# Optimization experiments

Hardware: AMD Instinct MI355X
Metric: run time of the kernel (lower is better)

Reference implementation:

```python
import jax, jax.numpy as jnp
import numpy as np
import math

D_MODEL = 1024
N_HEADS = 16
SLOT_DIM = 64
N_SLOTS = 1024
TOP_K = 2
LN_EPS = 1e-5


def setup_inputs() -> dict:
    key = jax.random.key(0)
    ks = jax.random.split(key, 8)
    x = jax.random.normal(ks[0], (4, 2048, D_MODEL), dtype=jnp.float32)
    ln_gamma = jnp.ones((D_MODEL,), jnp.float32)
    ln_beta = jnp.zeros((D_MODEL,), jnp.float32)
    q_w = jax.random.normal(ks[1], (N_HEADS * SLOT_DIM, D_MODEL), jnp.float32) / math.sqrt(D_MODEL)
    q_b = jnp.zeros((N_HEADS * SLOT_DIM,), jnp.float32)
    slot_signatures = jax.random.normal(ks[2], (N_HEADS, N_SLOTS, SLOT_DIM), jnp.float32) * 0.5
    slot_values = jax.random.normal(ks[3], (N_HEADS, N_SLOTS, SLOT_DIM), jnp.float32) * 0.02
    out_w = jax.random.normal(ks[4], (D_MODEL, N_HEADS * SLOT_DIM), jnp.float32) / math.sqrt(N_HEADS * SLOT_DIM)
    out_b = jnp.zeros((D_MODEL,), jnp.float32)
    temperature = jnp.ones((1,), jnp.float32)
    return {"x": x, "ln_gamma": ln_gamma, "ln_beta": ln_beta, "q_w": q_w, "q_b": q_b,
            "slot_signatures": slot_signatures, "slot_values": slot_values,
            "out_w": out_w, "out_b": out_b, "temperature": temperature}


def _ternary_ste(sig):
    # forward = {-1,0,+1} quantization; backward = identity (straight-through)
    q = jnp.where(sig > 0.3, 1.0, jnp.where(sig < -0.3, -1.0, 0.0))
    return sig + jax.lax.stop_gradient(q - sig)


def reference(x, ln_gamma, ln_beta, q_w, q_b, slot_signatures, slot_values, out_w, out_b, temperature):
    B, T, D = x.shape
    # LayerNorm
    mean = jnp.mean(x, axis=-1, keepdims=True)
    var = jnp.var(x, axis=-1, keepdims=True)
    x_norm = (x - mean) * jax.lax.rsqrt(var + LN_EPS) * ln_gamma + ln_beta
    # Query projection -> [B, T, H, slot_dim]
    q = (x_norm @ q_w.T + q_b).reshape(B, T, N_HEADS, SLOT_DIM)
    sigs = _ternary_ste(slot_signatures)  # [H, S, d]
    scores = jnp.einsum('bthd,hsd->bths', q, sigs)
    scores = scores / (temperature * math.sqrt(SLOT_DIM))  # [B, T, H, S]
    # top-k routing
    topk_scores, slot_idx = jax.lax.top_k(scores, TOP_K)  # [B, T, H, K]
    weights = jax.nn.softmax(topk_scores, axis=-1)
    # gather selected slot values: [B, T, H, K, d]
    h_idx = jnp.arange(N_HEADS)[None, None, :, None]
    selected = slot_values[h_idx, slot_idx]
    read = jnp.sum(selected * weights[..., None], axis=3)  # [B, T, H, d]
    read = read.reshape(B, T, N_HEADS * SLOT_DIM)
    out = read @ out_w.T + out_b
    return x + out
```

## Files before the change

### kernel.cpp

```cpp
#include <hip/hip_runtime.h>

typedef unsigned short u16;
typedef unsigned int   u32;
typedef float f32x4  __attribute__((ext_vector_type(4)));
typedef float f32x16 __attribute__((ext_vector_type(16)));
typedef __bf16 bf16x8 __attribute__((ext_vector_type(8)));

__device__ __forceinline__ u16 f2bf(float f){
  u32 u = __float_as_uint(f);
  u += 0x7fffu + ((u >> 16) & 1u);
  return (u16)(u >> 16);
}

__device__ __forceinline__ void gld16(const void* g, void* l){
  __builtin_amdgcn_global_load_lds((const __attribute__((address_space(1))) u32*)g,
                                   (__attribute__((address_space(3))) u32*)l, 16, 0, 0);
}

#define WAITCNT_VM0   0x0F70
#define WAITCNT_VM4   0x0F74
#define WAITCNT_LGKM0 0xC07F

__global__ __launch_bounds__(256) void convert_kernel(
    const float* __restrict__ qw, const float* __restrict__ ow,
    const float* __restrict__ sg,
    u16* __restrict__ qwb, u16* __restrict__ owb, u16* __restrict__ sgb){
  int i = (blockIdx.x * 256 + threadIdx.x) * 4;
  f32x4 a = *(const f32x4*)(qw + i);
  f32x4 b = *(const f32x4*)(ow + i);
  f32x4 s = *(const f32x4*)(sg + i);
  uint2 pa, pb, ps;
  pa.x = (u32)f2bf(a[0]) | ((u32)f2bf(a[1]) << 16);
  pa.y = (u32)f2bf(a[2]) | ((u32)f2bf(a[3]) << 16);
  pb.x = (u32)f2bf(b[0]) | ((u32)f2bf(b[1]) << 16);
  pb.y = (u32)f2bf(b[2]) | ((u32)f2bf(b[3]) << 16);
  float t0 = (s[0] > 0.3f) ? 1.0f : ((s[0] < -0.3f) ? -1.0f : 0.0f);
  float t1 = (s[1] > 0.3f) ? 1.0f : ((s[1] < -0.3f) ? -1.0f : 0.0f);
  float t2 = (s[2] > 0.3f) ? 1.0f : ((s[2] < -0.3f) ? -1.0f : 0.0f);
  float t3 = (s[3] > 0.3f) ? 1.0f : ((s[3] < -0.3f) ? -1.0f : 0.0f);
  ps.x = (u32)f2bf(t0) | ((u32)f2bf(t1) << 16);
  ps.y = (u32)f2bf(t2) | ((u32)f2bf(t3) << 16);
  *(uint2*)(qwb + i) = pa;
  *(uint2*)(owb + i) = pb;
  *(uint2*)(sgb + i) = ps;
}

__global__ __launch_bounds__(256) void ln_kernel(
    const float* __restrict__ x, const float* __restrict__ g,
    const float* __restrict__ b, u16* __restrict__ xn){
  const int tid = threadIdx.x, lane = tid & 63, w = tid >> 6;
  const int t = blockIdx.x * 4 + w;
  const float* xr = x + (size_t)t * 1024;
  f32x4 v[4];
  #pragma unroll
  for (int j = 0; j < 4; ++j) v[j] = *(const f32x4*)(xr + j * 256 + lane * 4);
  float s = 0.f, ss = 0.f;
  #pragma unroll
  for (int j = 0; j < 4; ++j)
    #pragma unroll
    for (int e = 0; e < 4; ++e){ s += v[j][e]; ss += v[j][e] * v[j][e]; }
  #pragma unroll
  for (int off = 32; off; off >>= 1){
    s  += __shfl_xor(s, off);
    ss += __shfl_xor(ss, off);
  }
  float mean = s * (1.0f / 1024.0f);
  float var  = ss * (1.0f / 1024.0f) - mean * mean;
  float rs   = rsqrtf(var + 1e-5f);
  #pragma unroll
  for (int j = 0; j < 4; ++j){
    f32x4 gv = *(const f32x4*)(g + j * 256 + lane * 4);
    f32x4 bv = *(const f32x4*)(b + j * 256 + lane * 4);
    float y0 = (v[j][0]-mean)*rs*gv[0]+bv[0];
    float y1 = (v[j][1]-mean)*rs*gv[1]+bv[1];
    float y2 = (v[j][2]-mean)*rs*gv[2]+bv[2];
    float y3 = (v[j][3]-mean)*rs*gv[3]+bv[3];
    uint2 pk;
    pk.x = (u32)f2bf(y0) | ((u32)f2bf(y1) << 16);
    pk.y = (u32)f2bf(y2) | ((u32)f2bf(y3) << 16);
    *(uint2*)(xn + (size_t)t * 1024 + j * 256 + lane * 4) = pk;
  }
}

__global__ __launch_bounds__(256, 2) void gemm_bt(
    const u16* __restrict__ A, const u16* __restrict__ B,
    const float* __restrict__ bias, const float* __restrict__ resid,
    float* __restrict__ outf, u16* __restrict__ outb, int mode){
  __shared__ u16 As[2][128 * 64];
  __shared__ u16 Bs[2][128 * 64];
  const int tid = threadIdx.x;
  const int b = blockIdx.x;
  const int m0 = ((b & 7) * 8 + ((b >> 3) & 7)) * 128;
  const int n0 = (b >> 6) * 128;
  const int w = tid >> 6, lane = tid & 63, lm = lane & 15, quad = lane >> 4;
  const int wm = (w & 1) * 64, wn = (w >> 1) * 64;
  const int lr = lane >> 3;
  const int lg = (lane & 7) ^ lr;
  const f32x4 fz = {0.f, 0.f, 0.f, 0.f};
  f32x4 acc[4][4];
  #pragma unroll
  for (int i = 0; i < 4; ++i)
    #pragma unroll
    for (int j = 0; j < 4; ++j) acc[i][j] = fz;

  const u16* gA = A + (size_t)(m0 + w * 32 + lr) * 1024 + lg * 8;
  const u16* gB = B + (size_t)(n0 + w * 32 + lr) * 1024 + lg * 8;
  const int lbase = (w * 32) * 64;
  const int sw = lm & 7;

  auto stage = [&](int kt, int bb){
    #pragma unroll
    for (int sub = 0; sub < 4; ++sub){
      gld16(gA + (size_t)(sub * 8) * 1024 + kt * 64, &As[bb][lbase + sub * 8 * 64]);
      gld16(gB + (size_t)(sub * 8) * 1024 + kt * 64, &Bs[bb][lbase + sub * 8 * 64]);
    }
  };

  stage(0, 0);
  for (int kt = 0; kt < 16; ++kt){
    __syncthreads();
    if (kt < 15) stage(kt + 1, (kt + 1) & 1);
    const u16* as = As[kt & 1];
    const u16* bs = Bs[kt & 1];
    #pragma unroll
    for (int kk = 0; kk < 2; ++kk){
      const int ch = ((quad + kk * 4) ^ sw) * 8;
      bf16x8 afr[4], bfr[4];
      #pragma unroll
      for (int i = 0; i < 4; ++i)
        afr[i] = *(const bf16x8*)(&as[(wm + i * 16 + lm) * 64 + ch]);
      #pragma unroll
      for (int j = 0; j < 4; ++j)
        bfr[j] = *(const bf16x8*)(&bs[(wn + j * 16 + lm) * 64 + ch]);
      #pragma unroll
      for (int i = 0; i < 4; ++i)
        #pragma unroll
        for (int j = 0; j < 4; ++j)
          acc[i][j] = __builtin_amdgcn_mfma_f32_16x16x32_bf16(afr[i], bfr[j], acc[i][j], 0, 0, 0);
    }
  }

  #pragma unroll
  for (int i = 0; i < 4; ++i){
    #pragma unroll
    for (int r = 0; r < 4; ++r){
      int grow = m0 + wm + i * 16 + quad * 4 + r;
      #pragma unroll
      for (int j = 0; j < 4; ++j){
        int gcol = n0 + wn + j * 16 + lm;
        float v = acc[i][j][r] + bias[gcol];
        if (mode){
          v += resid[(size_t)grow * 1024 + gcol];
          outf[(size_t)grow * 1024 + gcol] = v;
        } else {
          outb[(size_t)grow * 1024 + gcol] = f2bf(v);
        }
      }
    }
  }
}

#define MERGE2(V1,I1,V2,I2, o1,oi1,o2,oi2) {                      \
    u32   cb2 = (o2 > V2) ? oi2 : I2;                             \
    float c2  = fmaxf(V2, o2);                                    \
    u32   nb1 = (o1 > V1) ? oi1 : I1;                             \
    float n1  = fmaxf(V1, o1);                                    \
    float n2  = __builtin_amdgcn_fmed3f(V1, o1, c2);              \
    u32   nb2 = (n2 == o1) ? oi1 : ((n2 == V1) ? I1 : cb2);       \
    V1 = n1; I1 = nb1; V2 = n2; I2 = nb2; }

__global__ __launch_bounds__(256) void route_kernel(
    const u16* __restrict__ q, const u16* __restrict__ sig,
    const float* __restrict__ V, const float* __restrict__ temp,
    u16* __restrict__ rd){
  const int h = blockIdx.y;
  const int t0 = blockIdx.x * 64;
  const int tid = threadIdx.x, w = tid >> 6, lane = tid & 63;
  const int col = lane & 31, half = lane >> 5;

  __shared__ u16 sbuf[4][2][32 * 64];
  __shared__ float sv1[4][64], sv2[4][64];
  __shared__ u32   si1[4][64], si2[4][64];
  __shared__ float fw1[64], fw2[64];
  __shared__ int   fi1[64], fi2[64];

  const u16* q0 = q + (size_t)(t0 + col) * 1024 + h * 64 + half * 8;
  bf16x8 qa[4], qb[4];
  #pragma unroll
  for (int c = 0; c < 4; ++c){
    qa[c] = *(const bf16x8*)(q0 + c * 16);
    qb[c] = *(const bf16x8*)(q0 + 32 * 1024 + c * 16);
  }
  __builtin_amdgcn_s_waitcnt(WAITCNT_VM0);

  const int lr = lane >> 3, lg = (lane & 7) ^ lr;
  const u16* ssrc = sig + (size_t)h * 65536 + (size_t)(w * 256 + lr) * 64 + lg * 8;
  auto stage = [&](int i, int bb){
    const u16* s0 = ssrc + (size_t)i * 32 * 64;
    u16* d0 = &sbuf[w][bb][0];
    #pragma unroll
    for (int sub = 0; sub < 4; ++sub)
      gld16(s0 + sub * 8 * 64, d0 + sub * 8 * 64);
  };

  int p[4];
  #pragma unroll
  for (int c = 0; c < 4; ++c) p[c] = col * 64 + (((2 * c + half) ^ (col & 7)) * 8);

  const f32x16 fzero = {};
  float v1a = -3.0e38f, v2a = -3.0e38f, v1b = -3.0e38f, v2b = -3.0e38f;
  u32 b1a = 0, b2a = 0, b1b = 0, b2b = 0;

  stage(0, 0);
  stage(1, 1);
  #pragma unroll
  for (int i = 0; i < 8; ++i){
    if (i < 7) __builtin_amdgcn_s_waitcnt(WAITCNT_VM4);
    else       __builtin_amdgcn_s_waitcnt(WAITCNT_VM0);
    const u16* buf = sbuf[w][i & 1];
    bf16x8 sf0 = *(const bf16x8*)(&buf[p[0]]);
    bf16x8 sf1 = *(const bf16x8*)(&buf[p[1]]);
    bf16x8 sf2 = *(const bf16x8*)(&buf[p[2]]);
    bf16x8 sf3 = *(const bf16x8*)(&buf[p[3]]);
    __builtin_amdgcn_s_waitcnt(WAITCNT_LGKM0);
    if (i < 6) stage(i + 2, i & 1);
    u32 bt = (u32)i;
    #pragma unroll
    for (int set = 0; set < 2; ++set){
      f32x16 acc;
      acc = __builtin_amdgcn_mfma_f32_32x32x16_bf16(sf0, set ? qb[0] : qa[0], fzero, 0, 0, 0);
      acc = __builtin_amdgcn_mfma_f32_32x32x16_bf16(sf1, set ? qb[1] : qa[1], acc, 0, 0, 0);
      acc = __builtin_amdgcn_mfma_f32_32x32x16_bf16(sf2, set ? qb[2] : qa[2], acc, 0, 0, 0);
      acc = __builtin_amdgcn_mfma_f32_32x32x16_bf16(sf3, set ? qb[3] : qa[3], acc, 0, 0, 0);
      float k[16];
      #pragma unroll
      for (int r = 0; r < 16; ++r){
        u32 rk = (u32)((r & 3) + 8 * (r >> 2) + 4 * half);
        k[r] = __uint_as_float((__float_as_uint(acc[r]) & 0xFFFFFFE0u) | rk);
      }
      float h1[8], h2[8];
      #pragma unroll
      for (int j = 0; j < 8; ++j){
        h1[j] = fmaxf(k[2*j], k[2*j+1]);
        h2[j] = fminf(k[2*j], k[2*j+1]);
      }
      float g1[4], g2[4];
      #pragma unroll
      for (int j = 0; j < 4; ++j){
        g1[j] = fmaxf(h1[2*j], h1[2*j+1]);
        g2[j] = __builtin_amdgcn_fmed3f(h1[2*j], h1[2*j+1], fmaxf(h2[2*j], h2[2*j+1]));
      }
      float e1[2], e2[2];
      #pragma unroll
      for (int j = 0; j < 2; ++j){
        e1[j] = fmaxf(g1[2*j], g1[2*j+1]);
        e2[j] = __builtin_amdgcn_fmed3f(g1[2*j], g1[2*j+1], fmaxf(g2[2*j], g2[2*j+1]));
      }
      float m1 = fmaxf(e1[0], e1[1]);
      float m2 = __builtin_amdgcn_fmed3f(e1[0], e1[1], fmaxf(e2[0], e2[1]));
      if (set){ MERGE2(v1b, b1b, v2b, b2b, m1, bt, m2, bt); }
      else    { MERGE2(v1a, b1a, v2a, b2a, m1, bt, m2, bt); }
    }
  }

  #pragma unroll
  for (int set = 0; set < 2; ++set){
    float v1 = set ? v1b : v1a, v2 = set ? v2b : v2a;
    u32   b1 = set ? b1b : b1a, b2 = set ? b2b : b2a;
    float o1 = __shfl_xor(v1, 32);
    float o2 = __shfl_xor(v2, 32);
    u32 ob1 = (u32)__shfl_xor((int)b1, 32);
    u32 ob2 = (u32)__shfl_xor((int)b2, 32);
    MERGE2(v1, b1, v2, b2, o1, ob1, o2, ob2);
    if (half == 0){
      int tk = set * 32 + col;
      sv1[w][tk] = v1; sv2[w][tk] = v2;
      si1[w][tk] = (u32)(w * 256) + b1 * 32 + (__float_as_uint(v1) & 31u);
      si2[w][tk] = (u32)(w * 256) + b2 * 32 + (__float_as_uint(v2) & 31u);
    }
  }
  __syncthreads();

  if (tid < 64){
    float V1 = sv1[0][tid], V2 = sv2[0][tid];
    u32   I1 = si1[0][tid], I2 = si2[0][tid];
    #pragma unroll
    for (int ws = 1; ws < 4; ++ws){
      float o1 = sv1[ws][tid], o2 = sv2[ws][tid];
      u32  oi1 = si1[ws][tid], oi2 = si2[ws][tid];
      MERGE2(V1, I1, V2, I2, o1, oi1, o2, oi2);
    }
    float s1 = __uint_as_float(__float_as_uint(V1) & 0xFFFFFFE0u);
    float s2 = __uint_as_float(__float_as_uint(V2) & 0xFFFFFFE0u);
    float tsc = 1.0f / (temp[0] * 8.0f);
    float ex = __expf((s2 - s1) * tsc);
    float iw = 1.0f / (1.0f + ex);
    fw1[tid] = iw; fw2[tid] = ex * iw;
    fi1[tid] = (int)I1; fi2[tid] = (int)I2;
  }
  __syncthreads();

  int tl = tid >> 2, d0 = (tid & 3) * 16;
  const float* va = V + ((size_t)h * 1024 + fi1[tl]) * 64 + d0;
  const float* vb = V + ((size_t)h * 1024 + fi2[tl]) * 64 + d0;
  float W1 = fw1[tl], W2 = fw2[tl];
  u16* dst = rd + (size_t)(t0 + tl) * 1024 + h * 64 + d0;
  #pragma unroll
  for (int g = 0; g < 2; ++g){
    f32x4 xa = *(const f32x4*)(va + g * 8);
    f32x4 xb = *(const f32x4*)(va + g * 8 + 4);
    f32x4 ya = *(const f32x4*)(vb + g * 8);
    f32x4 yb = *(const f32x4*)(vb + g * 8 + 4);
    uint4 o;
    o.x = (u32)f2bf(W1*xa[0]+W2*ya[0]) | ((u32)f2bf(W1*xa[1]+W2*ya[1]) << 16);
    o.y = (u32)f2bf(W1*xa[2]+W2*ya[2]) | ((u32)f2bf(W1*xa[3]+W2*ya[3]) << 16);
    o.z = (u32)f2bf(W1*xb[0]+W2*yb[0]) | ((u32)f2bf(W1*xb[1]+W2*yb[1]) << 16);
    o.w = (u32)f2bf(W1*xb[2]+W2*yb[2]) | ((u32)f2bf(W1*xb[3]+W2*yb[3]) << 16);
    *(uint4*)(dst + g * 8) = o;
  }
}

extern "C" void kernel_launch(void* const* d_in, const int* in_sizes, int n_in,
                              void* d_out, int out_size, void* d_ws, size_t ws_size,
                              hipStream_t stream){
  const float* x    = (const float*)d_in[0];
  const float* lng  = (const float*)d_in[1];
  const float* lnb  = (const float*)d_in[2];
  const float* qw   = (const float*)d_in[3];
  const float* qb   = (const float*)d_in[4];
  const float* sig  = (const float*)d_in[5];
  const float* sv   = (const float*)d_in[6];
  const float* ow   = (const float*)d_in[7];
  const float* ob   = (const float*)d_in[8];
  const float* temp = (const float*)d_in[9];
  float* out = (float*)d_out;

  char* ws = (char*)d_ws;
  u16* xn   = (u16*)(ws);
  u16* qwb  = (u16*)(ws + 16777216);
  u16* owb  = (u16*)(ws + 16777216 + 2097152);
  u16* sgb  = (u16*)(ws + 16777216 + 2 * 2097152);
  u16* qb16 = (u16*)(ws + 16777216 + 3 * 2097152);
  u16* rdb  = xn;

  convert_kernel<<<1024, 256, 0, stream>>>(qw, ow, sig, qwb, owb, sgb);
  ln_kernel<<<2048, 256, 0, stream>>>(x, lng, lnb, xn);
  gemm_bt<<<512, 256, 0, stream>>>(xn, qwb, qb, nullptr, nullptr, qb16, 0);
  route_kernel<<<dim3(128, 16), 256, 0, stream>>>(qb16, sgb, sv, temp, rdb);
  gemm_bt<<<512, 256, 0, stream>>>(rdb, owb, ob, x, out, nullptr, 1);
}
```

Measured before the change: 210.7 us.

## Keep slot signatures register-resident and loop over token tiles in routing kernel

The routing kernel is restructured so each 512-thread block owns one head and 256 tokens. Each of 8 waves holds a 128-slot slice of the ternary signatures in registers for the whole block, instead of streaming all signatures through LDS for every 64-token block. Query tiles are prefetched one step ahead, and the per-wave top-2 candidates are merged through a double-buffered LDS packet with one barrier per 32-token step. The in-register top-2 reduction tree is regrouped into triples. This cuts signature reloads and LDS staging, but raises register pressure and adds a barrier each token step.

```diff
diff --git a/kernel.cpp b/kernel.cpp
--- a/kernel.cpp
+++ b/kernel.cpp
@@ -16,10 +16,6 @@
   __builtin_amdgcn_global_load_lds((const __attribute__((address_space(1))) u32*)g,
                                    (__attribute__((address_space(3))) u32*)l, 16, 0, 0);
 }
-
-#define WAITCNT_VM0   0x0F70
-#define WAITCNT_VM4   0x0F74
-#define WAITCNT_LGKM0 0xC07F
 
 __global__ __launch_bounds__(256) void convert_kernel(
     const float* __restrict__ qw, const float* __restrict__ ow,
@@ -169,154 +165,123 @@
     u32   nb2 = (n2 == o1) ? oi1 : ((n2 == V1) ? I1 : cb2);       \
     V1 = n1; I1 = nb1; V2 = n2; I2 = nb2; }
 
-__global__ __launch_bounds__(256) void route_kernel(
+__global__ __launch_bounds__(512) void route2_kernel(
     const u16* __restrict__ q, const u16* __restrict__ sig,
     const float* __restrict__ V, const float* __restrict__ temp,
     u16* __restrict__ rd){
-  const int h = blockIdx.y;
-  const int t0 = blockIdx.x * 64;
+  const int b = blockIdx.x;
+  const int h = b & 15, chunk = b >> 4;
+  const int t0 = chunk * 256;
   const int tid = threadIdx.x, w = tid >> 6, lane = tid & 63;
   const int col = lane & 31, half = lane >> 5;
 
-  __shared__ u16 sbuf[4][2][32 * 64];
-  __shared__ float sv1[4][64], sv2[4][64];
-  __shared__ u32   si1[4][64], si2[4][64];
-  __shared__ float fw1[64], fw2[64];
-  __shared__ int   fi1[64], fi2[64];
-
-  const u16* q0 = q + (size_t)(t0 + col) * 1024 + h * 64 + half * 8;
-  bf16x8 qa[4], qb[4];
-  #pragma unroll
-  for (int c = 0; c < 4; ++c){
-    qa[c] = *(const bf16x8*)(q0 + c * 16);
-    qb[c] = *(const bf16x8*)(q0 + 32 * 1024 + c * 16);
-  }
-  __builtin_amdgcn_s_waitcnt(WAITCNT_VM0);
-
-  const int lr = lane >> 3, lg = (lane & 7) ^ lr;
-  const u16* ssrc = sig + (size_t)h * 65536 + (size_t)(w * 256 + lr) * 64 + lg * 8;
-  auto stage = [&](int i, int bb){
-    const u16* s0 = ssrc + (size_t)i * 32 * 64;
-    u16* d0 = &sbuf[w][bb][0];
-    #pragma unroll
-    for (int sub = 0; sub < 4; ++sub)
-      gld16(s0 + sub * 8 * 64, d0 + sub * 8 * 64);
-  };
-
-  int p[4];
-  #pragma unroll
-  for (int c = 0; c < 4; ++c) p[c] = col * 64 + (((2 * c + half) ^ (col & 7)) * 8);
+  __shared__ uint4 sv[2][8][32];
+
+  const float tsc = 1.0f / (temp[0] * 8.0f);
+
+  const u16* sigh = sig + (size_t)h * 65536;
+  bf16x8 sfr[4][4];
+  #pragma unroll
+  for (int blk = 0; blk < 4; ++blk){
+    const u16* sp = sigh + (size_t)(w * 128 + blk * 32 + col) * 64 + half * 8;
+    #pragma unroll
+    for (int c = 0; c < 4; ++c)
+      sfr[blk][c] = *(const bf16x8*)(sp + c * 16);
+  }
+
+  u32 rk[16];
+  #pragma unroll
+  for (int r = 0; r < 16; ++r) rk[r] = (u32)((r & 3) + 8 * (r >> 2) + 4 * half);
+
+  const u16* qbase = q + (size_t)h * 64 + half * 8;
+  bf16x8 qf[4], qn[4];
+  {
+    const u16* qp = qbase + (size_t)(t0 + col) * 1024;
+    #pragma unroll
+    for (int c = 0; c < 4; ++c) qf[c] = *(const bf16x8*)(qp + c * 16);
+  }
 
   const f32x16 fzero = {};
-  float v1a = -3.0e38f, v2a = -3.0e38f, v1b = -3.0e38f, v2b = -3.0e38f;
-  u32 b1a = 0, b2a = 0, b1b = 0, b2b = 0;
-
-  stage(0, 0);
-  stage(1, 1);
-  #pragma unroll
-  for (int i = 0; i < 8; ++i){
-    if (i < 7) __builtin_amdgcn_s_waitcnt(WAITCNT_VM4);
-    else       __builtin_amdgcn_s_waitcnt(WAITCNT_VM0);
-    const u16* buf = sbuf[w][i & 1];
-    bf16x8 sf0 = *(const bf16x8*)(&buf[p[0]]);
-    bf16x8 sf1 = *(const bf16x8*)(&buf[p[1]]);
-    bf16x8 sf2 = *(const bf16x8*)(&buf[p[2]]);
-    bf16x8 sf3 = *(const bf16x8*)(&buf[p[3]]);
-    __builtin_amdgcn_s_waitcnt(WAITCNT_LGKM0);
-    if (i < 6) stage(i + 2, i & 1);
-    u32 bt = (u32)i;
-    #pragma unroll
-    for (int set = 0; set < 2; ++set){
+  for (int tt = 0; tt < 8; ++tt){
+    {
+      int tn = (tt < 7) ? tt + 1 : 7;
+      const u16* qp = qbase + (size_t)(t0 + tn * 32 + col) * 1024;
+      #pragma unroll
+      for (int c = 0; c < 4; ++c) qn[c] = *(const bf16x8*)(qp + c * 16);
+    }
+    float v1 = -3.0e38f, v2 = -3.0e38f; u32 i1 = 0, i2 = 0;
+    #pragma unroll
+    for (int blk = 0; blk < 4; ++blk){
       f32x16 acc;
-      acc = __builtin_amdgcn_mfma_f32_32x32x16_bf16(sf0, set ? qb[0] : qa[0], fzero, 0, 0, 0);
-      acc = __builtin_amdgcn_mfma_f32_32x32x16_bf16(sf1, set ? qb[1] : qa[1], acc, 0, 0, 0);
-      acc = __builtin_amdgcn_mfma_f32_32x32x16_bf16(sf2, set ? qb[2] : qa[2], acc, 0, 0, 0);
-      acc = __builtin_amdgcn_mfma_f32_32x32x16_bf16(sf3, set ? qb[3] : qa[3], acc, 0, 0, 0);
+      acc = __builtin_amdgcn_mfma_f32_32x32x16_bf16(sfr[blk][0], qf[0], fzero, 0, 0, 0);
+      acc = __builtin_amdgcn_mfma_f32_32x32x16_bf16(sfr[blk][1], qf[1], acc, 0, 0, 0);
+      acc = __builtin_amdgcn_mfma_f32_32x32x16_bf16(sfr[blk][2], qf[2], acc, 0, 0, 0);
+      acc = __builtin_amdgcn_mfma_f32_32x32x16_bf16(sfr[blk][3], qf[3], acc, 0, 0, 0);
       float k[16];
       #pragma unroll
-      for (int r = 0; r < 16; ++r){
-        u32 rk = (u32)((r & 3) + 8 * (r >> 2) + 4 * half);
-        k[r] = __uint_as_float((__float_as_uint(acc[r]) & 0xFFFFFFE0u) | rk);
+      for (int r = 0; r < 16; ++r)
+        k[r] = __uint_as_float((__float_as_uint(acc[r]) & 0xFFFFFFE0u) | rk[r]);
+      float a1[5], a2[5];
+      #pragma unroll
+      for (int i = 0; i < 5; ++i){
+        float x = k[3*i], y = k[3*i+1], z = k[3*i+2];
+        a1[i] = fmaxf(fmaxf(x, y), z);
+        a2[i] = __builtin_amdgcn_fmed3f(x, y, z);
       }
-      float h1[8], h2[8];
-      #pragma unroll
-      for (int j = 0; j < 8; ++j){
-        h1[j] = fmaxf(k[2*j], k[2*j+1]);
-        h2[j] = fminf(k[2*j], k[2*j+1]);
-      }
-      float g1[4], g2[4];
-      #pragma unroll
-      for (int j = 0; j < 4; ++j){
-        g1[j] = fmaxf(h1[2*j], h1[2*j+1]);
-        g2[j] = __builtin_amdgcn_fmed3f(h1[2*j], h1[2*j+1], fmaxf(h2[2*j], h2[2*j+1]));
-      }
-      float e1[2], e2[2];
-      #pragma unroll
-      for (int j = 0; j < 2; ++j){
-        e1[j] = fmaxf(g1[2*j], g1[2*j+1]);
-        e2[j] = __builtin_amdgcn_fmed3f(g1[2*j], g1[2*j+1], fmaxf(g2[2*j], g2[2*j+1]));
-      }
-      float m1 = fmaxf(e1[0], e1[1]);
-      float m2 = __builtin_amdgcn_fmed3f(e1[0], e1[1], fmaxf(e2[0], e2[1]));
-      if (set){ MERGE2(v1b, b1b, v2b, b2b, m1, bt, m2, bt); }
-      else    { MERGE2(v1a, b1a, v2a, b2a, m1, bt, m2, bt); }
-    }
-  }
-
-  #pragma unroll
-  for (int set = 0; set < 2; ++set){
-    float v1 = set ? v1b : v1a, v2 = set ? v2b : v2a;
-    u32   b1 = set ? b1b : b1a, b2 = set ? b2b : b2a;
-    float o1 = __shfl_xor(v1, 32);
-    float o2 = __shfl_xor(v2, 32);
-    u32 ob1 = (u32)__shfl_xor((int)b1, 32);
-    u32 ob2 = (u32)__shfl_xor((int)b2, 32);
-    MERGE2(v1, b1, v2, b2, o1, ob1, o2, ob2);
+      float m1 = fmaxf(a1[0], a1[1]);
+      float m2 = __builtin_amdgcn_fmed3f(a1[0], a1[1], fmaxf(a2[0], a2[1]));
+      float n1 = fmaxf(a1[2], a1[3]);
+      float n2 = __builtin_amdgcn_fmed3f(a1[2], a1[3], fmaxf(a2[2], a2[3]));
+      float o1 = fmaxf(a1[4], k[15]);
+      float o2 = __builtin_amdgcn_fmed3f(a1[4], k[15], a2[4]);
+      float p1 = fmaxf(m1, n1);
+      float p2 = __builtin_amdgcn_fmed3f(m1, n1, fmaxf(m2, n2));
+      float f1 = fmaxf(p1, o1);
+      float f2 = __builtin_amdgcn_fmed3f(p1, o1, fmaxf(p2, o2));
+      u32 bt = (u32)blk;
+      MERGE2(v1, i1, v2, i2, f1, bt, f2, bt);
+    }
+    #pragma unroll
+    for (int c = 0; c < 4; ++c) qf[c] = qn[c];
+    {
+      float x1 = __shfl_xor(v1, 32);
+      float x2 = __shfl_xor(v2, 32);
+      u32 xi1 = (u32)__shfl_xor((int)i1, 32);
+      u32 xi2 = (u32)__shfl_xor((int)i2, 32);
+      MERGE2(v1, i1, v2, i2, x1, xi1, x2, xi2);
+    }
     if (half == 0){
-      int tk = set * 32 + col;
-      sv1[w][tk] = v1; sv2[w][tk] = v2;
-      si1[w][tk] = (u32)(w * 256) + b1 * 32 + (__float_as_uint(v1) & 31u);
-      si2[w][tk] = (u32)(w * 256) + b2 * 32 + (__float_as_uint(v2) & 31u);
-    }
-  }
-  __syncthreads();
-
-  if (tid < 64){
-    float V1 = sv1[0][tid], V2 = sv2[0][tid];
-    u32   I1 = si1[0][tid], I2 = si2[0][tid];
-    #pragma unroll
-    for (int ws = 1; ws < 4; ++ws){
-      float o1 = sv1[ws][tid], o2 = sv2[ws][tid];
-      u32  oi1 = si1[ws][tid], oi2 = si2[ws][tid];
-      MERGE2(V1, I1, V2, I2, o1, oi1, o2, oi2);
-    }
-    float s1 = __uint_as_float(__float_as_uint(V1) & 0xFFFFFFE0u);
-    float s2 = __uint_as_float(__float_as_uint(V2) & 0xFFFFFFE0u);
-    float tsc = 1.0f / (temp[0] * 8.0f);
-    float ex = __expf((s2 - s1) * tsc);
+      uint4 pkt;
+      pkt.x = __float_as_uint(v1);
+      pkt.y = __float_as_uint(v2);
+      pkt.z = (u32)(w * 128) + i1 * 32 + (__float_as_uint(v1) & 31u);
+      pkt.w = (u32)(w * 128) + i2 * 32 + (__float_as_uint(v2) & 31u);
+      sv[tt & 1][w][col] = pkt;
+    }
+    __syncthreads();
+    int tk = w * 4 + (lane >> 4);
+    uint4 pa = sv[tt & 1][0][tk];
+    float V1 = __uint_as_float(pa.x), V2 = __uint_as_float(pa.y);
+    u32 I1 = pa.z, I2 = pa.w;
+    #pragma unroll
+    for (int ws = 1; ws < 8; ++ws){
+      uint4 pb = sv[tt & 1][ws][tk];
+      float q1 = __uint_as_float(pb.x), q2 = __uint_as_float(pb.y);
+      u32 j1 = pb.z, j2 = pb.w;
+      MERGE2(V1, I1, V2, I2, q1, j1, q2, j2);
+    }
+    float sc1 = __uint_as_float(__float_as_uint(V1) & 0xFFFFFFE0u);
+    float sc2 = __uint_as_float(__float_as_uint(V2) & 0xFFFFFFE0u);
+    float ex = __expf((sc2 - sc1) * tsc);
     float iw = 1.0f / (1.0f + ex);
-    fw1[tid] = iw; fw2[tid] = ex * iw;
-    fi1[tid] = (int)I1; fi2[tid] = (int)I2;
-  }
-  __syncthreads();
-
-  int tl = tid >> 2, d0 = (tid & 3) * 16;
-  const float* va = V + ((size_t)h * 1024 + fi1[tl]) * 64 + d0;
-  const float* vb = V + ((size_t)h * 1024 + fi2[tl]) * 64 + d0;
-  float W1 = fw1[tl], W2 = fw2[tl];
-  u16* dst = rd + (size_t)(t0 + tl) * 1024 + h * 64 + d0;
-  #pragma unroll
-  for (int g = 0; g < 2; ++g){
-    f32x4 xa = *(const f32x4*)(va + g * 8);
-    f32x4 xb = *(const f32x4*)(va + g * 8 + 4);
-    f32x4 ya = *(const f32x4*)(vb + g * 8);
-    f32x4 yb = *(const f32x4*)(vb + g * 8 + 4);
-    uint4 o;
-    o.x = (u32)f2bf(W1*xa[0]+W2*ya[0]) | ((u32)f2bf(W1*xa[1]+W2*ya[1]) << 16);
-    o.y = (u32)f2bf(W1*xa[2]+W2*ya[2]) | ((u32)f2bf(W1*xa[3]+W2*ya[3]) << 16);
-    o.z = (u32)f2bf(W1*xb[0]+W2*yb[0]) | ((u32)f2bf(W1*xb[1]+W2*yb[1]) << 16);
-    o.w = (u32)f2bf(W1*xb[2]+W2*yb[2]) | ((u32)f2bf(W1*xb[3]+W2*yb[3]) << 16);
-    *(uint4*)(dst + g * 8) = o;
+    float W1 = iw, W2 = ex * iw;
+    int token = t0 + tt * 32 + tk, d0 = (lane & 15) * 4;
+    f32x4 xa = *(const f32x4*)(V + ((size_t)h * 1024 + I1) * 64 + d0);
+    f32x4 xb = *(const f32x4*)(V + ((size_t)h * 1024 + I2) * 64 + d0);
+    uint2 o;
+    o.x = (u32)f2bf(W1*xa[0]+W2*xb[0]) | ((u32)f2bf(W1*xa[1]+W2*xb[1]) << 16);
+    o.y = (u32)f2bf(W1*xa[2]+W2*xb[2]) | ((u32)f2bf(W1*xa[3]+W2*xb[3]) << 16);
+    *(uint2*)(rd + (size_t)token * 1024 + h * 64 + d0) = o;
   }
 }
 
@@ -346,6 +311,6 @@
   convert_kernel<<<1024, 256, 0, stream>>>(qw, ow, sig, qwb, owb, sgb);
   ln_kernel<<<2048, 256, 0, stream>>>(x, lng, lnb, xn);
   gemm_bt<<<512, 256, 0, stream>>>(xn, qwb, qb, nullptr, nullptr, qb16, 0);
-  route_kernel<<<dim3(128, 16), 256, 0, stream>>>(qb16, sgb, sv, temp, rdb);
+  route2_kernel<<<512, 512, 0, stream>>>(qb16, sgb, sv, temp, rdb);
   gemm_bt<<<512, 256, 0, stream>>>(rdb, owb, ob, x, out, nullptr, 1);
 }
```

Measured after the change: 212.1 us. About the same (+0.7%).
